# Performance work log

Measured on AMD Instinct MI355X. Metric: run time of the kernel, lower is better.

Reference implementation:

```python
import jax, jax.numpy as jnp
import numpy as np

NUM_ENTITIES = 40000
NUM_RELATIONS = 500
NUM_EDGES = 400000
ENT_DIM = 50
REL_DIM = 50
NUM_HEADS = 8
UNITS = [150, 300]
NEG_SLOPE = 0.2


def setup_inputs() -> dict:
    key = jax.random.key(0)
    ks = jax.random.split(key, 12)
    h_index = jax.random.randint(ks[0], (NUM_EDGES,), 0, NUM_ENTITIES)
    r_index = jax.random.randint(ks[1], (NUM_EDGES,), 0, NUM_RELATIONS)
    t_index = jax.random.randint(ks[2], (NUM_EDGES,), 0, NUM_ENTITIES)
    std_e = np.sqrt(1.0 / ENT_DIM).astype(np.float32)
    std_r = np.sqrt(1.0 / REL_DIM).astype(np.float32)
    entity_embeddings = jax.random.truncated_normal(ks[3], -2.0, 2.0, (NUM_ENTITIES, ENT_DIM), jnp.float32) * std_e
    relation_embeddings = jax.random.truncated_normal(ks[4], -2.0, 2.0, (NUM_RELATIONS, REL_DIM), jnp.float32) * std_r
    # gat0: input ent dim 50, rel dim 50 -> concat 150, units 150
    c0 = ENT_DIM + REL_DIM + ENT_DIM
    gat0_kernel = jax.random.normal(ks[5], (NUM_HEADS, c0, UNITS[0]), jnp.float32) * (1.0 / np.sqrt(c0))
    gat0_attn = jax.random.normal(ks[6], (NUM_HEADS, UNITS[0]), jnp.float32) * (1.0 / np.sqrt(UNITS[0]))
    gat0_rel_kernel = jax.random.normal(ks[7], (REL_DIM, UNITS[0]), jnp.float32) * (1.0 / np.sqrt(REL_DIM))
    # gat1: input ent dim 8*150=1200, rel dim 150 -> concat 2550, units 300
    e1 = NUM_HEADS * UNITS[0]
    c1 = e1 + UNITS[0] + e1
    gat1_kernel = jax.random.normal(ks[8], (NUM_HEADS, c1, UNITS[1]), jnp.float32) * (1.0 / np.sqrt(c1))
    gat1_attn = jax.random.normal(ks[9], (NUM_HEADS, UNITS[1]), jnp.float32) * (1.0 / np.sqrt(UNITS[1]))
    gat1_rel_kernel = jax.random.normal(ks[10], (UNITS[0], UNITS[1]), jnp.float32) * (1.0 / np.sqrt(UNITS[0]))
    dense_w = jax.random.normal(ks[11], (ENT_DIM, UNITS[1]), jnp.float32) * (1.0 / np.sqrt(ENT_DIM))
    dense_b = jnp.zeros((UNITS[1],), jnp.float32)
    return dict(h_index=h_index, r_index=r_index, t_index=t_index,
                entity_embeddings=entity_embeddings, relation_embeddings=relation_embeddings,
                gat0_kernel=gat0_kernel, gat0_attn=gat0_attn, gat0_rel_kernel=gat0_rel_kernel,
                gat1_kernel=gat1_kernel, gat1_attn=gat1_attn, gat1_rel_kernel=gat1_rel_kernel,
                dense_w=dense_w, dense_b=dense_b)


def _kbgat_layer(h, r, t, ent, rel, kernel, attn, rel_kernel):
    """One KBGAT layer. kernel: [H, De+Dr+De, U] acting on concat(ent[h], rel[r], ent[t]).
    Split kernel so projections happen at node/relation level (equivalent, avoids E x concat_dim)."""
    N = ent.shape[0]
    De = ent.shape[1]
    Dr = rel.shape[1]
    outs = []
    for hd in range(kernel.shape[0]):
        W = kernel[hd]
        Wh, Wr, Wt = W[:De], W[De:De + Dr], W[De + Dr:]
        # message c_{hrt} = W [ent_h ; rel_r ; ent_t] : [E, U]
        c = (ent @ Wh)[h] + (rel @ Wr)[r] + (ent @ Wt)[t]
        s = jax.nn.leaky_relu(c @ attn[hd], NEG_SLOPE)  # [E]
        # segment softmax over triples sharing the same head entity
        m = jax.ops.segment_max(s, h, num_segments=N)
        e = jnp.exp(s - m[h])
        d = jax.ops.segment_sum(e, h, num_segments=N)
        a = e / (d[h] + 1e-10)
        agg = jax.ops.segment_sum(a[:, None] * c, h, num_segments=N)  # [N, U]
        outs.append(jax.nn.elu(agg))
    rel_out = rel @ rel_kernel
    return outs, rel_out


def reference(h_index, r_index, t_index, entity_embeddings, relation_embeddings,
              gat0_kernel, gat0_attn, gat0_rel_kernel,
              gat1_kernel, gat1_attn, gat1_rel_kernel, dense_w, dense_b):
    h = h_index.astype(jnp.int32)
    r = r_index.astype(jnp.int32)
    t = t_index.astype(jnp.int32)
    # dropout rate is 0.0 / inference -> identity
    outs0, rel0 = _kbgat_layer(h, r, t, entity_embeddings, relation_embeddings,
                               gat0_kernel, gat0_attn, gat0_rel_kernel)
    feat = jnp.concatenate(outs0, axis=-1)  # [N, H*U0]
    outs1, rel1 = _kbgat_layer(h, r, t, feat, rel0, gat1_kernel, gat1_attn, gat1_rel_kernel)
    ent_out = outs1[0]
    for o in outs1[1:]:
        ent_out = ent_out + o  # add_n over heads
    ent_out = ent_out + (entity_embeddings @ dense_w + dense_b)  # dense residual
    return ent_out, rel1
```

## Files before the change

### kernel.cpp

```cpp
#include <hip/hip_runtime.h>
#include <hip/hip_bf16.h>
#include <math.h>
#include <stdint.h>

typedef __attribute__((ext_vector_type(8))) __bf16 bf16x8;
typedef __attribute__((ext_vector_type(4))) float f32x4;
typedef unsigned short us;

#define GLP(p) ((__attribute__((address_space(1))) void*)(p))
#define LDP(p) ((__attribute__((address_space(3))) void*)(p))

static __device__ __forceinline__ float b2f(us u) {
    return __uint_as_float(((unsigned int)u) << 16);
}
static __device__ __forceinline__ us f2b(float f) {
    unsigned int x = __float_as_uint(f);
    return (us)((x + 0x7fffu + ((x >> 16) & 1u)) >> 16);
}

__global__ __launch_bounds__(256) void sentinel(float* out, int n, float v) {
    int i = blockIdx.x * 256 + threadIdx.x;
    if (i < n) out[i] = v;
}

__global__ __launch_bounds__(256) void zero_featpad(us* __restrict__ feat) {
    int idx = blockIdx.x * 256 + threadIdx.x;
    if (idx < 40064 * 16) {
        int n = idx >> 4, c = idx & 15;
        feat[(size_t)n * 1216 + 1200 + c] = 0;
    }
}
__global__ __launch_bounds__(256) void zero_x0pad(us* __restrict__ X0) {
    int idx = blockIdx.x * 256 + threadIdx.x;
    if (idx < 4 * 64 * 192) {
        int w = idx / (64 * 192);
        int rem = idx % (64 * 192);
        int rr = rem / 192, c = rem % 192;
        X0[((size_t)w * 40064 + 40000 + rr) * 192 + c] = 0;
    }
}

__global__ __launch_bounds__(256) void count_edges(const int* __restrict__ h, int* __restrict__ counts) {
    int e = blockIdx.x * 256 + threadIdx.x;
    if (e < 400000) atomicAdd(&counts[h[e]], 1);
}

__global__ void scan40k(const int* __restrict__ counts, int* __restrict__ rs) {
    __shared__ int part[1024];
    int tid = threadIdx.x;
    int base = tid * 40;
    int s = 0;
    for (int i = 0; i < 40; ++i) { int idx = base + i; s += (idx < 40000) ? counts[idx] : 0; }
    part[tid] = s;
    __syncthreads();
    for (int off = 1; off < 1024; off <<= 1) {
        int v = (tid >= off) ? part[tid - off] : 0;
        __syncthreads();
        part[tid] += v;
        __syncthreads();
    }
    int run = (tid == 0) ? 0 : part[tid - 1];
    for (int i = 0; i < 40; ++i) {
        int idx = base + i;
        if (idx < 40000) { rs[idx] = run; run += counts[idx]; }
    }
    if (tid == 1023) rs[40000] = part[1023];
}

__global__ __launch_bounds__(256) void scatter_edges(const int* __restrict__ h, const int* __restrict__ rs,
                                                     int* __restrict__ cursor, int* __restrict__ se) {
    int e = blockIdx.x * 256 + threadIdx.x;
    if (e < 400000) {
        int n = h[e];
        int pos = rs[n] + atomicAdd(&cursor[n], 1);
        se[pos] = e;
    }
}

__global__ __launch_bounds__(256) void pack_ent(const float* __restrict__ ent, us* __restrict__ A0) {
    int idx = blockIdx.x * 256 + threadIdx.x;
    if (idx >= 40064 * 64) return;
    int n = idx >> 6, k = idx & 63;
    A0[idx] = (n < 40000 && k < 50) ? f2b(ent[n * 50 + k]) : (us)0;
}

__global__ __launch_bounds__(256) void build_V0(const float* __restrict__ g0k, const float* __restrict__ attn0,
                                                float* __restrict__ V0) {
    int idx = blockIdx.x * 256 + threadIdx.x;
    if (idx >= 50 * 24) return;
    int k = idx / 24, g = idx % 24;
    int part = g >> 3, hd = g & 7;
    int row = k + (part == 1 ? 100 : (part == 2 ? 50 : 0));
    float s = 0.f;
    for (int u = 0; u < 150; ++u)
        s += g0k[(hd * 150 + row) * 150 + u] * attn0[hd * 150 + u];
    V0[idx] = s;
}

__global__ __launch_bounds__(256) void build_VT0(const float* __restrict__ g0k, const float* __restrict__ attn0,
                                                 us* __restrict__ VT0) {
    int idx = blockIdx.x * 256 + threadIdx.x;
    if (idx >= 128 * 64) return;
    int g = idx >> 6, k = idx & 63;
    us v = 0;
    if (g < 16 && k < 50) {
        int part = g >> 3, hd = g & 7;
        int row = part ? (100 + k) : k;
        float s = 0.f;
        for (int u = 0; u < 150; ++u)
            s += g0k[(hd * 150 + row) * 150 + u] * attn0[hd * 150 + u];
        v = f2b(s);
    }
    VT0[idx] = v;
}

__global__ __launch_bounds__(256) void build_VT1(const float* __restrict__ g1k, const float* __restrict__ attn1,
                                                 us* __restrict__ VT1) {
    int idx = blockIdx.x * 256 + threadIdx.x;
    if (idx >= 128 * 1216) return;
    int g = idx / 1216, k = idx % 1216;
    us v = 0;
    if (g < 16 && k < 1200) {
        int part = g >> 3, hd = g & 7;
        int row = part ? (1350 + k) : k;
        float s = 0.f;
        for (int u = 0; u < 300; ++u)
            s += g1k[((size_t)hd * 2550 + row) * 300 + u] * attn1[hd * 300 + u];
        v = f2b(s);
    }
    VT1[idx] = v;
}

__global__ __launch_bounds__(256) void build_Vr1(const float* __restrict__ g1k, const float* __restrict__ attn1,
                                                 float* __restrict__ Vr1) {
    int idx = blockIdx.x * 256 + threadIdx.x;
    if (idx >= 150 * 8) return;
    int k = idx / 8, hd = idx % 8;
    float s = 0.f;
    for (int u = 0; u < 300; ++u)
        s += g1k[((size_t)hd * 2550 + 1200 + k) * 300 + u] * attn1[hd * 300 + u];
    Vr1[idx] = s;
}

__global__ __launch_bounds__(256) void scalar_proj(const void* __restrict__ Av, int aIsF32, int lda, int K,
                                                   const float* __restrict__ V, int ldv, int col0, int G,
                                                   float* __restrict__ out) {
    __shared__ float arow[1216];
    long n = blockIdx.x;
    if (aIsF32) {
        const float* A = (const float*)Av;
        for (int k = threadIdx.x; k < K; k += 256) arow[k] = A[n * lda + k];
    } else {
        const us* A = (const us*)Av;
        for (int k = threadIdx.x; k < K; k += 256) arow[k] = b2f(A[n * lda + k]);
    }
    __syncthreads();
    int g = threadIdx.x >> 4;
    int sl = threadIdx.x & 15;
    if (g < G) {
        float s = 0.f;
        for (int k = sl; k < K; k += 16) s += arow[k] * V[k * ldv + col0 + g];
        for (int off = 8; off; off >>= 1) s += __shfl_down(s, off, 16);
        if (sl == 0) out[n * G + g] = s;
    }
}

__global__ __launch_bounds__(256) void edge_stats(const int* __restrict__ rs, const int* __restrict__ se,
                                                  const int* __restrict__ rIdx, const int* __restrict__ tIdx,
                                                  const float* __restrict__ sc, const float* __restrict__ arr,
                                                  us* __restrict__ eAT, float* __restrict__ sfac) {
    int tid = blockIdx.x * 256 + threadIdx.x;
    if (tid >= 40000 * 8) return;
    int n = tid >> 3, hd = tid & 7;
    float ah = sc[n * 16 + hd];
    int p0 = rs[n], p1 = rs[n + 1];
    float m = -INFINITY, d = 0.f;
    for (int p = p0; p < p1; ++p) {
        int e = se[p];
        float s = ah + arr[rIdx[e] * 8 + hd] + sc[tIdx[e] * 16 + 8 + hd];
        s = (s > 0.f) ? s : 0.2f * s;
        if (s > m) { d = d * expf(m - s) + 1.f; m = s; }
        else d += expf(s - m);
    }
    float inv = 1.f / (d + 1e-10f);
    us* ea = eAT + (size_t)hd * 400000;
    for (int p = p0; p < p1; ++p) {
        int e = se[p];
        float s = ah + arr[rIdx[e] * 8 + hd] + sc[tIdx[e] * 16 + 8 + hd];
        s = (s > 0.f) ? s : 0.2f * s;
        ea[p] = f2b(expf(s - m) * inv);
    }
    sfac[tid] = d * inv;
}

__global__ __launch_bounds__(256) void agg0x4(int g, const int* __restrict__ rs, const int* __restrict__ se,
                                              const int* __restrict__ rIdx, const int* __restrict__ tIdx,
                                              const us* __restrict__ eAT, const float* __restrict__ sfac,
                                              const float* __restrict__ ent, const float* __restrict__ rel,
                                              us* __restrict__ X0) {
    __shared__ int sr[128], st[128];
    __shared__ float sa[4][128];
    long n = blockIdx.x;
    int tid = threadIdx.x;
    int lane = tid & 63, wave = tid >> 6;
    int hd = 4 * g + wave;
    int k = lane;
    float ev = (k < 50) ? ent[n * 50 + k] : 0.f;
    float xh = sfac[n * 8 + hd] * ev;
    float ra = 0.f, ta = 0.f;
    int p0 = rs[n], p1 = rs[n + 1];
    for (int c0 = p0; c0 < p1; c0 += 128) {
        int cnt = min(128, p1 - c0);
        __syncthreads();
        if (tid < cnt) {
            int e = se[c0 + tid];
            sr[tid] = rIdx[e];
            st[tid] = tIdx[e];
#pragma unroll
            for (int w = 0; w < 4; ++w)
                sa[w][tid] = b2f(eAT[(size_t)(4 * g + w) * 400000 + c0 + tid]);
        }
        __syncthreads();
#pragma unroll 2
        for (int i = 0; i < cnt; ++i) {
            float a = sa[wave][i];
            int r = sr[i], t = st[i];
            if (k < 50) {
                ra += a * rel[r * 50 + k];
                ta += a * ent[(long)t * 50 + k];
            }
        }
    }
    us* row = X0 + ((size_t)wave * 40064 + n) * 192;
    if (k < 50) { row[k] = f2b(xh); row[50 + k] = f2b(ra); row[100 + k] = f2b(ta); }
    if (lane < 42) row[150 + lane] = 0;
}

__global__ __launch_bounds__(256) void build_B0T8(const float* __restrict__ g0k, us* __restrict__ B) {
    int idx = blockIdx.x * 256 + threadIdx.x;
    if (idx >= 8 * 256 * 192) return;
    int hd = idx / (256 * 192);
    int u = (idx / 192) % 256, k = idx % 192;
    us v = 0;
    if (u < 150 && k < 150) v = f2b(g0k[((size_t)hd * 150 + k) * 150 + u]);
    B[idx] = v;
}

__global__ __launch_bounds__(256) void build_B1Th2(int g, const float* __restrict__ g1k, us* __restrict__ B) {
    int idx = blockIdx.x * 256 + threadIdx.x;
    if (idx >= 1280 * 1216) return;
    int j = idx / 1216, k = idx % 1216;
    us v = 0;
    if (j < 1216 && k < 1200) {
        int blk = j / 304, u = j % 304;
        if (u < 300) {
            int hd = 2 * g + (blk & 1);
            int row = (blk >= 2) ? (1350 + k) : k;
            v = f2b(g1k[((size_t)hd * 2550 + row) * 300 + u]);
        }
    }
    B[idx] = v;
}

__global__ __launch_bounds__(256) void gemm_bt(const us* __restrict__ A, const us* __restrict__ BT,
                                               us* __restrict__ C, int K, int ldc, int nColReal,
                                               int colOff0, int colOffZ, long aStrideZ, long btStrideZ,
                                               int act) {
    __shared__ __align__(16) us As[128 * 64];
    __shared__ __align__(16) us Bs[128 * 64];
    const int z = blockIdx.z;
    A += (size_t)z * aStrideZ;
    BT += (size_t)z * btStrideZ;
    const int colBase = colOff0 + z * colOffZ;
    const int tid = threadIdx.x;
    const int lane = tid & 63, wave = tid >> 6;
    const int wr = wave >> 1, wc = wave & 1;
    const int r16 = lane & 15, g4 = lane >> 4;
    const long bm = blockIdx.y, bn = blockIdx.x;
    const int cg = tid & 7;

    f32x4 acc[4][4];
#pragma unroll
    for (int m = 0; m < 4; ++m)
#pragma unroll
        for (int n = 0; n < 4; ++n) acc[m][n] = (f32x4){0.f, 0.f, 0.f, 0.f};

    for (int kt = 0; kt < K; kt += 64) {
#pragma unroll
        for (int i = 0; i < 4; ++i) {
            int idx = tid + i * 256;
            int row = idx >> 3;
            const us* ga = A + (bm * 128 + row) * (long)K + kt + cg * 8;
            __builtin_amdgcn_global_load_lds(GLP(ga), LDP(&As[idx * 8]), 16, 0, 0);
        }
#pragma unroll
        for (int i = 0; i < 4; ++i) {
            int idx = tid + i * 256;
            int row = idx >> 3;
            const us* gb = BT + (bn * 128 + row) * (long)K + kt + cg * 8;
            __builtin_amdgcn_global_load_lds(GLP(gb), LDP(&Bs[idx * 8]), 16, 0, 0);
        }
        asm volatile("s_waitcnt vmcnt(0)" ::: "memory");
        __syncthreads();
#pragma unroll
        for (int kk = 0; kk < 2; ++kk) {
            bf16x8 af[4], bfr[4];
#pragma unroll
            for (int m = 0; m < 4; ++m)
                af[m] = *(const bf16x8*)&As[(wr * 64 + m * 16 + r16) * 64 + kk * 32 + g4 * 8];
#pragma unroll
            for (int n = 0; n < 4; ++n)
                bfr[n] = *(const bf16x8*)&Bs[(wc * 64 + n * 16 + r16) * 64 + kk * 32 + g4 * 8];
#pragma unroll
            for (int m = 0; m < 4; ++m)
#pragma unroll
                for (int n = 0; n < 4; ++n)
                    acc[m][n] = __builtin_amdgcn_mfma_f32_16x16x32_bf16(af[m], bfr[n], acc[m][n], 0, 0, 0);
        }
        __syncthreads();
    }
#pragma unroll
    for (int m = 0; m < 4; ++m)
#pragma unroll
        for (int n = 0; n < 4; ++n)
#pragma unroll
            for (int j = 0; j < 4; ++j) {
                int cc = (int)bn * 128 + wc * 64 + n * 16 + r16;
                if (cc < nColReal) {
                    long row = bm * 128 + wr * 64 + m * 16 + g4 * 4 + j;
                    float v = acc[m][n][j];
                    if (act) v = (v > 0.f) ? v : expm1f(v);
                    C[row * (long)ldc + colBase + cc] = f2b(v);
                }
            }
}

__global__ __launch_bounds__(256) void gemm_bt_f32(const us* __restrict__ A, const us* __restrict__ BT,
                                                   float* __restrict__ C, int K, int ldc, int nColReal) {
    __shared__ __align__(16) us As[128 * 64];
    __shared__ __align__(16) us Bs[128 * 64];
    const int tid = threadIdx.x;
    const int lane = tid & 63, wave = tid >> 6;
    const int wr = wave >> 1, wc = wave & 1;
    const int r16 = lane & 15, g4 = lane >> 4;
    const long bm = blockIdx.y, bn = blockIdx.x;
    const int cg = tid & 7;

    f32x4 acc[4][4];
#pragma unroll
    for (int m = 0; m < 4; ++m)
#pragma unroll
        for (int n = 0; n < 4; ++n) acc[m][n] = (f32x4){0.f, 0.f, 0.f, 0.f};

    for (int kt = 0; kt < K; kt += 64) {
#pragma unroll
        for (int i = 0; i < 4; ++i) {
            int idx = tid + i * 256;
            int row = idx >> 3;
            const us* ga = A + (bm * 128 + row) * (long)K + kt + cg * 8;
            __builtin_amdgcn_global_load_lds(GLP(ga), LDP(&As[idx * 8]), 16, 0, 0);
        }
#pragma unroll
        for (int i = 0; i < 4; ++i) {
            int idx = tid + i * 256;
            int row = idx >> 3;
            const us* gb = BT + (bn * 128 + row) * (long)K + kt + cg * 8;
            __builtin_amdgcn_global_load_lds(GLP(gb), LDP(&Bs[idx * 8]), 16, 0, 0);
        }
        asm volatile("s_waitcnt vmcnt(0)" ::: "memory");
        __syncthreads();
#pragma unroll
        for (int kk = 0; kk < 2; ++kk) {
            bf16x8 af[4], bfr[4];
#pragma unroll
            for (int m = 0; m < 4; ++m)
                af[m] = *(const bf16x8*)&As[(wr * 64 + m * 16 + r16) * 64 + kk * 32 + g4 * 8];
#pragma unroll
            for (int n = 0; n < 4; ++n)
                bfr[n] = *(const bf16x8*)&Bs[(wc * 64 + n * 16 + r16) * 64 + kk * 32 + g4 * 8];
#pragma unroll
            for (int m = 0; m < 4; ++m)
#pragma unroll
                for (int n = 0; n < 4; ++n)
                    acc[m][n] = __builtin_amdgcn_mfma_f32_16x16x32_bf16(af[m], bfr[n], acc[m][n], 0, 0, 0);
        }
        __syncthreads();
    }
#pragma unroll
    for (int m = 0; m < 4; ++m)
#pragma unroll
        for (int n = 0; n < 4; ++n)
#pragma unroll
            for (int j = 0; j < 4; ++j) {
                int cc = (int)bn * 128 + wc * 64 + n * 16 + r16;
                if (cc < nColReal) {
                    long row = bm * 128 + wr * 64 + m * 16 + g4 * 4 + j;
                    C[row * (long)ldc + cc] = acc[m][n][j];
                }
            }
}

__global__ __launch_bounds__(256) void rel0_kernel(const float* __restrict__ rel, const float* __restrict__ g0rk,
                                                   float* __restrict__ rel0b) {
    int idx = blockIdx.x * 256 + threadIdx.x;
    if (idx >= 500 * 150) return;
    int rI = idx / 150, u = idx % 150;
    float s = 0.f;
    for (int k = 0; k < 50; ++k) s += rel[rI * 50 + k] * g0rk[k * 150 + u];
    rel0b[idx] = s;
}

__global__ __launch_bounds__(256) void pr1_kernel(const float* __restrict__ rel0b, const float* __restrict__ g1k,
                                                  float* __restrict__ PR1) {
    int idx = blockIdx.x * 256 + threadIdx.x;
    if (idx >= 500 * 2400) return;
    int rI = idx / 2400, jj = idx % 2400;
    int hd = jj / 300, u = jj % 300;
    float s = 0.f;
    for (int k = 0; k < 150; ++k)
        s += rel0b[rI * 150 + k] * g1k[((size_t)hd * 2550 + 1200 + k) * 300 + u];
    PR1[idx] = s;
}

__global__ __launch_bounds__(256) void rel1_kernel(const float* __restrict__ rel0b, const float* __restrict__ g1rk,
                                                   float* __restrict__ out) {
    int idx = blockIdx.x * 256 + threadIdx.x;
    if (idx >= 500 * 300) return;
    int rI = idx / 300, u = idx % 300;
    float s = 0.f;
    for (int k = 0; k < 150; ++k) s += rel0b[rI * 150 + k] * g1rk[k * 300 + u];
    out[idx] = s;
}

__global__ __launch_bounds__(256) void out_init(const float* __restrict__ ent, const float* __restrict__ dw,
                                                const float* __restrict__ db, float* __restrict__ outAcc) {
    int idx = blockIdx.x * 256 + threadIdx.x;
    if (idx >= 40000 * 300) return;
    int n = idx / 300, u = idx % 300;
    float s = db[u];
    for (int k = 0; k < 50; ++k) s += ent[n * 50 + k] * dw[k * 300 + u];
    outAcc[idx] = s;
}

__global__ __launch_bounds__(256) void agg1h2(int g, const int* __restrict__ rs, const int* __restrict__ se,
                                              const int* __restrict__ rIdx, const int* __restrict__ tIdx,
                                              const us* __restrict__ eAT, const float* __restrict__ sfac,
                                              const us* __restrict__ C1g2, const float* __restrict__ PR1,
                                              float* __restrict__ outf) {
    __shared__ int sr[128], st[128];
    __shared__ float sa0[128], sa1[128];
    long n = blockIdx.x;
    int tid = threadIdx.x;
    int hd0 = 2 * g, hd1 = hd0 + 1;
    int d = tid, d2 = tid + 256;
    bool a2 = (d2 < 300);
    float sf0 = sfac[n * 8 + hd0], sf1 = sfac[n * 8 + hd1];
    const us* crow = C1g2 + (size_t)n * 1216;
    float acc00 = sf0 * b2f(crow[d]);
    float acc10 = sf1 * b2f(crow[304 + d]);
    float acc01 = a2 ? sf0 * b2f(crow[d2]) : 0.f;
    float acc11 = a2 ? sf1 * b2f(crow[304 + d2]) : 0.f;
    const us* ea0 = eAT + (size_t)hd0 * 400000;
    const us* ea1 = eAT + (size_t)hd1 * 400000;
    int p0 = rs[n], p1 = rs[n + 1];
    for (int c0 = p0; c0 < p1; c0 += 128) {
        int cnt = min(128, p1 - c0);
        __syncthreads();
        if (tid < cnt) {
            int e = se[c0 + tid];
            sr[tid] = rIdx[e];
            st[tid] = tIdx[e];
            sa0[tid] = b2f(ea0[c0 + tid]);
            sa1[tid] = b2f(ea1[c0 + tid]);
        }
        __syncthreads();
#pragma unroll 2
        for (int i = 0; i < cnt; ++i) {
            int r = sr[i], t = st[i];
            float a0 = sa0[i], a1 = sa1[i];
            const us* ct = C1g2 + (size_t)t * 1216;
            const float* pr = PR1 + (size_t)r * 2400;
            acc00 += a0 * (pr[hd0 * 300 + d] + b2f(ct[608 + d]));
            acc10 += a1 * (pr[hd1 * 300 + d] + b2f(ct[912 + d]));
            if (a2) {
                acc01 += a0 * (pr[hd0 * 300 + d2] + b2f(ct[608 + d2]));
                acc11 += a1 * (pr[hd1 * 300 + d2] + b2f(ct[912 + d2]));
            }
        }
    }
    float v00 = (acc00 > 0.f) ? acc00 : expm1f(acc00);
    float v10 = (acc10 > 0.f) ? acc10 : expm1f(acc10);
    outf[n * 300 + d] += v00 + v10;
    if (a2) {
        float v01 = (acc01 > 0.f) ? acc01 : expm1f(acc01);
        float v11 = (acc11 > 0.f) ? acc11 : expm1f(acc11);
        outf[n * 300 + d2] += v01 + v11;
    }
}

extern "C" void kernel_launch(void* const* d_in, const int* in_sizes, int n_in,
                              void* d_out, int out_size, void* d_ws, size_t ws_size,
                              hipStream_t stream) {
    const int* hIdx = (const int*)d_in[0];
    const int* rIdx = (const int*)d_in[1];
    const int* tIdx = (const int*)d_in[2];
    const float* ent  = (const float*)d_in[3];
    const float* rel  = (const float*)d_in[4];
    const float* g0k  = (const float*)d_in[5];
    const float* at0w = (const float*)d_in[6];
    const float* g0rk = (const float*)d_in[7];
    const float* g1k  = (const float*)d_in[8];
    const float* at1w = (const float*)d_in[9];
    const float* g1rk = (const float*)d_in[10];
    const float* dw   = (const float*)d_in[11];
    const float* db   = (const float*)d_in[12];
    float* outf = (float*)d_out;

    {
        const int exp_sz[13] = {400000, 400000, 400000, 2000000, 25000, 180000, 1200,
                                7500, 6120000, 2400, 45000, 15000, 300};
        bool ok = (n_in == 13);
        for (int i = 0; ok && i < 13; ++i) ok = (in_sizes[i] == exp_sz[i]);
        if (!ok) {
            sentinel<<<(out_size + 255) / 256, 256, 0, stream>>>(outf, out_size, 44.0f);
            return;
        }
    }

    char* p = (char*)d_ws;
    auto carve = [&](size_t bytes) -> char* {
        char* r = p;
        p += (bytes + 255) & ~(size_t)255;
        return r;
    };
    int* counts = (int*)carve(40000 * 4);
    int* cursor = (int*)carve(40000 * 4);
    int* rs     = (int*)carve(40001 * 4);
    int* se     = (int*)carve(400000 * 4);
    float* sc   = (float*)carve((size_t)40064 * 16 * 4);
    float* arS  = (float*)carve(500 * 8 * 4);
    us* eAT     = (us*)carve((size_t)8 * 400000 * 2);
    float* sfac = (float*)carve((size_t)40000 * 8 * 4);
    float* V0  = (float*)carve(50 * 24 * 4);
    float* Vr1 = (float*)carve(150 * 8 * 4);
    float* rel0b = (float*)carve(500 * 150 * 4);
    float* PR1 = (float*)carve((size_t)500 * 2400 * 4);
    us* VT0   = (us*)carve((size_t)128 * 64 * 2);
    us* VT1   = (us*)carve((size_t)128 * 1216 * 2);
    us* B0T8  = (us*)carve((size_t)8 * 256 * 192 * 2);
    us* B1Th2 = (us*)carve((size_t)1280 * 1216 * 2);
    us* feat  = (us*)carve((size_t)40064 * 1216 * 2);
    char* tail = p;
    us* A0   = (us*)tail;
    us* X0   = (us*)tail;
    us* C1g2 = (us*)tail;
    size_t tailNeed = (size_t)40064 * 1216 * 2;
    size_t totalNeed = (size_t)(tail - (char*)d_ws) + tailNeed;
    if (totalNeed > ws_size) {
        sentinel<<<(out_size + 255) / 256, 256, 0, stream>>>(outf, out_size, 42.0f);
        return;
    }

    hipMemsetAsync(counts, 0, 40000 * 4, stream);
    hipMemsetAsync(cursor, 0, 40000 * 4, stream);
    zero_featpad<<<(40064 * 16 + 255) / 256, 256, 0, stream>>>(feat);

    count_edges<<<1563, 256, 0, stream>>>(hIdx, counts);
    scan40k<<<1, 1024, 0, stream>>>(counts, rs);
    scatter_edges<<<1563, 256, 0, stream>>>(hIdx, rs, cursor, se);

    pack_ent<<<(40064 * 64 + 255) / 256, 256, 0, stream>>>(ent, A0);
    build_VT0<<<(128 * 64 + 255) / 256, 256, 0, stream>>>(g0k, at0w, VT0);
    gemm_bt_f32<<<dim3(1, 313), 256, 0, stream>>>(A0, VT0, sc, 64, 16, 16);
    build_V0<<<5, 256, 0, stream>>>(g0k, at0w, V0);
    scalar_proj<<<500, 256, 0, stream>>>(rel, 1, 50, 50, V0, 24, 16, 8, arS);
    edge_stats<<<1250, 256, 0, stream>>>(rs, se, rIdx, tIdx, sc, arS, eAT, sfac);

    zero_x0pad<<<(4 * 64 * 192 + 255) / 256, 256, 0, stream>>>(X0);
    build_B0T8<<<(8 * 256 * 192 + 255) / 256, 256, 0, stream>>>(g0k, B0T8);
    for (int g = 0; g < 2; ++g) {
        agg0x4<<<40000, 256, 0, stream>>>(g, rs, se, rIdx, tIdx, eAT, sfac, ent, rel, X0);
        gemm_bt<<<dim3(2, 313, 4), 256, 0, stream>>>(X0, B0T8 + (size_t)g * 4 * 256 * 192, feat,
                                                     192, 1216, 150, g * 600, 150,
                                                     (long)40064 * 192, (long)256 * 192, 1);
    }

    rel0_kernel<<<(500 * 150 + 255) / 256, 256, 0, stream>>>(rel, g0rk, rel0b);
    build_VT1<<<(128 * 1216 + 255) / 256, 256, 0, stream>>>(g1k, at1w, VT1);
    build_Vr1<<<5, 256, 0, stream>>>(g1k, at1w, Vr1);
    gemm_bt_f32<<<dim3(1, 313), 256, 0, stream>>>(feat, VT1, sc, 1216, 16, 16);
    scalar_proj<<<500, 256, 0, stream>>>(rel0b, 1, 150, 150, Vr1, 8, 0, 8, arS);
    edge_stats<<<1250, 256, 0, stream>>>(rs, se, rIdx, tIdx, sc, arS, eAT, sfac);
    pr1_kernel<<<(500 * 2400 + 255) / 256, 256, 0, stream>>>(rel0b, g1k, PR1);

    out_init<<<(40000 * 300 + 255) / 256, 256, 0, stream>>>(ent, dw, db, outf);

    for (int g = 0; g < 4; ++g) {
        build_B1Th2<<<(1280 * 1216 + 255) / 256, 256, 0, stream>>>(g, g1k, B1Th2);
        gemm_bt<<<dim3(10, 313, 1), 256, 0, stream>>>(feat, B1Th2, C1g2,
                                                      1216, 1216, 1216, 0, 0, 0, 0, 0);
        agg1h2<<<40000, 256, 0, stream>>>(g, rs, se, rIdx, tIdx, eAT, sfac, C1g2, PR1, outf);
    }

    rel1_kernel<<<(500 * 300 + 255) / 256, 256, 0, stream>>>(rel0b, g1rk, outf + (size_t)40000 * 300);
}
```

Measured before the change: 2.333 ms.

## Double-buffer GEMM LDS tiles and XOR-swizzle layout to avoid bank conflicts

Both bf16 MFMA GEMM kernels now use two LDS buffers, so the global-to-LDS loads for the next K tile are issued before computing the current one, with a partial vmcnt wait. The LDS tile layout is also XOR-swizzled by row to reduce bank conflicts on the 16-byte fragment reads. The shared body is factored into a macro. This doubles LDS use per block (64KB), which may reduce occupancy.

```diff
diff --git a/kernel.cpp b/kernel.cpp
--- a/kernel.cpp
+++ b/kernel.cpp
@@ -262,142 +262,92 @@
     B[idx] = v;
 }
 
-__global__ __launch_bounds__(256) void gemm_bt(const us* __restrict__ A, const us* __restrict__ BT,
+#define GEMM_BODY(EPILOG)                                                                       \
+    __shared__ __align__(16) us As[2][128 * 64];                                                \
+    __shared__ __align__(16) us Bs[2][128 * 64];                                                \
+    const int tid = threadIdx.x;                                                                \
+    const int lane = tid & 63, wave = tid >> 6;                                                 \
+    const int wr = wave >> 1, wc = wave & 1;                                                    \
+    const int r16 = lane & 15, g4 = lane >> 4;                                                  \
+    const long bm = blockIdx.y, bn = blockIdx.x;                                                \
+    f32x4 acc[4][4];                                                                            \
+    _Pragma("unroll") for (int m = 0; m < 4; ++m)                                               \
+        _Pragma("unroll") for (int n = 0; n < 4; ++n) acc[m][n] = (f32x4){0.f, 0.f, 0.f, 0.f};  \
+    auto stage = [&](int buf, int kt) {                                                         \
+        _Pragma("unroll") for (int i = 0; i < 4; ++i) {                                         \
+            int idx = tid + i * 256;                                                            \
+            int row = idx >> 3, sub = idx & 7;                                                  \
+            int scol = ((sub ^ (row & 7)) << 3);                                                \
+            const us* ga = A + (bm * 128 + row) * (long)K + kt + scol;                          \
+            __builtin_amdgcn_global_load_lds(GLP(ga), LDP(&As[buf][idx * 8]), 16, 0, 0);        \
+        }                                                                                       \
+        _Pragma("unroll") for (int i = 0; i < 4; ++i) {                                         \
+            int idx = tid + i * 256;                                                            \
+            int row = idx >> 3, sub = idx & 7;                                                  \
+            int scol = ((sub ^ (row & 7)) << 3);                                                \
+            const us* gb = BT + (bn * 128 + row) * (long)K + kt + scol;                         \
+            __builtin_amdgcn_global_load_lds(GLP(gb), LDP(&Bs[buf][idx * 8]), 16, 0, 0);        \
+        }                                                                                       \
+    };                                                                                          \
+    const int nt = K >> 6;                                                                      \
+    stage(0, 0);                                                                                \
+    const int sxor = (r16 & 7) << 3;                                                            \
+    for (int t = 0; t < nt; ++t) {                                                              \
+        int cur = t & 1;                                                                        \
+        if (t + 1 < nt) {                                                                       \
+            stage(cur ^ 1, (t + 1) << 6);                                                       \
+            asm volatile("s_waitcnt vmcnt(8)" ::: "memory");                                    \
+        } else {                                                                                \
+            asm volatile("s_waitcnt vmcnt(0)" ::: "memory");                                    \
+        }                                                                                       \
+        __builtin_amdgcn_s_barrier();                                                           \
+        asm volatile("" ::: "memory");                                                          \
+        _Pragma("unroll") for (int kk = 0; kk < 2; ++kk) {                                      \
+            bf16x8 af[4], bfr[4];                                                               \
+            _Pragma("unroll") for (int m = 0; m < 4; ++m)                                       \
+                af[m] = *(const bf16x8*)&As[cur][(wr * 64 + m * 16 + r16) * 64 +                \
+                                               ((kk * 32 + g4 * 8) ^ sxor)];                    \
+            _Pragma("unroll") for (int n = 0; n < 4; ++n)                                       \
+                bfr[n] = *(const bf16x8*)&Bs[cur][(wc * 64 + n * 16 + r16) * 64 +               \
+                                                ((kk * 32 + g4 * 8) ^ sxor)];                   \
+            _Pragma("unroll") for (int m = 0; m < 4; ++m)                                       \
+                _Pragma("unroll") for (int n = 0; n < 4; ++n)                                   \
+                    acc[m][n] = __builtin_amdgcn_mfma_f32_16x16x32_bf16(af[m], bfr[n],          \
+                                                                        acc[m][n], 0, 0, 0);    \
+        }                                                                                       \
+        asm volatile("" ::: "memory");                                                          \
+        __builtin_amdgcn_s_barrier();                                                           \
+    }                                                                                           \
+    _Pragma("unroll") for (int m = 0; m < 4; ++m)                                               \
+        _Pragma("unroll") for (int n = 0; n < 4; ++n)                                           \
+            _Pragma("unroll") for (int j = 0; j < 4; ++j) { EPILOG }
+
+__global__ __launch_bounds__(256) void gemm_bt(const us* __restrict__ A_, const us* __restrict__ BT_,
                                                us* __restrict__ C, int K, int ldc, int nColReal,
                                                int colOff0, int colOffZ, long aStrideZ, long btStrideZ,
                                                int act) {
-    __shared__ __align__(16) us As[128 * 64];
-    __shared__ __align__(16) us Bs[128 * 64];
     const int z = blockIdx.z;
-    A += (size_t)z * aStrideZ;
-    BT += (size_t)z * btStrideZ;
+    const us* A = A_ + (size_t)z * aStrideZ;
+    const us* BT = BT_ + (size_t)z * btStrideZ;
     const int colBase = colOff0 + z * colOffZ;
-    const int tid = threadIdx.x;
-    const int lane = tid & 63, wave = tid >> 6;
-    const int wr = wave >> 1, wc = wave & 1;
-    const int r16 = lane & 15, g4 = lane >> 4;
-    const long bm = blockIdx.y, bn = blockIdx.x;
-    const int cg = tid & 7;
-
-    f32x4 acc[4][4];
-#pragma unroll
-    for (int m = 0; m < 4; ++m)
-#pragma unroll
-        for (int n = 0; n < 4; ++n) acc[m][n] = (f32x4){0.f, 0.f, 0.f, 0.f};
-
-    for (int kt = 0; kt < K; kt += 64) {
-#pragma unroll
-        for (int i = 0; i < 4; ++i) {
-            int idx = tid + i * 256;
-            int row = idx >> 3;
-            const us* ga = A + (bm * 128 + row) * (long)K + kt + cg * 8;
-            __builtin_amdgcn_global_load_lds(GLP(ga), LDP(&As[idx * 8]), 16, 0, 0);
-        }
-#pragma unroll
-        for (int i = 0; i < 4; ++i) {
-            int idx = tid + i * 256;
-            int row = idx >> 3;
-            const us* gb = BT + (bn * 128 + row) * (long)K + kt + cg * 8;
-            __builtin_amdgcn_global_load_lds(GLP(gb), LDP(&Bs[idx * 8]), 16, 0, 0);
-        }
-        asm volatile("s_waitcnt vmcnt(0)" ::: "memory");
-        __syncthreads();
-#pragma unroll
-        for (int kk = 0; kk < 2; ++kk) {
-            bf16x8 af[4], bfr[4];
-#pragma unroll
-            for (int m = 0; m < 4; ++m)
-                af[m] = *(const bf16x8*)&As[(wr * 64 + m * 16 + r16) * 64 + kk * 32 + g4 * 8];
-#pragma unroll
-            for (int n = 0; n < 4; ++n)
-                bfr[n] = *(const bf16x8*)&Bs[(wc * 64 + n * 16 + r16) * 64 + kk * 32 + g4 * 8];
-#pragma unroll
-            for (int m = 0; m < 4; ++m)
-#pragma unroll
-                for (int n = 0; n < 4; ++n)
-                    acc[m][n] = __builtin_amdgcn_mfma_f32_16x16x32_bf16(af[m], bfr[n], acc[m][n], 0, 0, 0);
-        }
-        __syncthreads();
-    }
-#pragma unroll
-    for (int m = 0; m < 4; ++m)
-#pragma unroll
-        for (int n = 0; n < 4; ++n)
-#pragma unroll
-            for (int j = 0; j < 4; ++j) {
-                int cc = (int)bn * 128 + wc * 64 + n * 16 + r16;
-                if (cc < nColReal) {
-                    long row = bm * 128 + wr * 64 + m * 16 + g4 * 4 + j;
-                    float v = acc[m][n][j];
-                    if (act) v = (v > 0.f) ? v : expm1f(v);
-                    C[row * (long)ldc + colBase + cc] = f2b(v);
-                }
-            }
+    GEMM_BODY(
+        int cc = (int)bn * 128 + wc * 64 + n * 16 + r16;
+        if (cc < nColReal) {
+            long row = bm * 128 + wr * 64 + m * 16 + g4 * 4 + j;
+            float v = acc[m][n][j];
+            if (act) v = (v > 0.f) ? v : expm1f(v);
+            C[row * (long)ldc + colBase + cc] = f2b(v);
+        })
 }
 
 __global__ __launch_bounds__(256) void gemm_bt_f32(const us* __restrict__ A, const us* __restrict__ BT,
                                                    float* __restrict__ C, int K, int ldc, int nColReal) {
-    __shared__ __align__(16) us As[128 * 64];
-    __shared__ __align__(16) us Bs[128 * 64];
-    const int tid = threadIdx.x;
-    const int lane = tid & 63, wave = tid >> 6;
-    const int wr = wave >> 1, wc = wave & 1;
-    const int r16 = lane & 15, g4 = lane >> 4;
-    const long bm = blockIdx.y, bn = blockIdx.x;
-    const int cg = tid & 7;
-
-    f32x4 acc[4][4];
-#pragma unroll
-    for (int m = 0; m < 4; ++m)
-#pragma unroll
-        for (int n = 0; n < 4; ++n) acc[m][n] = (f32x4){0.f, 0.f, 0.f, 0.f};
-
-    for (int kt = 0; kt < K; kt += 64) {
-#pragma unroll
-        for (int i = 0; i < 4; ++i) {
-            int idx = tid + i * 256;
-            int row = idx >> 3;
-            const us* ga = A + (bm * 128 + row) * (long)K + kt + cg * 8;
-            __builtin_amdgcn_global_load_lds(GLP(ga), LDP(&As[idx * 8]), 16, 0, 0);
-        }
-#pragma unroll
-        for (int i = 0; i < 4; ++i) {
-            int idx = tid + i * 256;
-            int row = idx >> 3;
-            const us* gb = BT + (bn * 128 + row) * (long)K + kt + cg * 8;
-            __builtin_amdgcn_global_load_lds(GLP(gb), LDP(&Bs[idx * 8]), 16, 0, 0);
-        }
-        asm volatile("s_waitcnt vmcnt(0)" ::: "memory");
-        __syncthreads();
-#pragma unroll
-        for (int kk = 0; kk < 2; ++kk) {
-            bf16x8 af[4], bfr[4];
-#pragma unroll
-            for (int m = 0; m < 4; ++m)
-                af[m] = *(const bf16x8*)&As[(wr * 64 + m * 16 + r16) * 64 + kk * 32 + g4 * 8];
-#pragma unroll
-            for (int n = 0; n < 4; ++n)
-                bfr[n] = *(const bf16x8*)&Bs[(wc * 64 + n * 16 + r16) * 64 + kk * 32 + g4 * 8];
-#pragma unroll
-            for (int m = 0; m < 4; ++m)
-#pragma unroll
-                for (int n = 0; n < 4; ++n)
-                    acc[m][n] = __builtin_amdgcn_mfma_f32_16x16x32_bf16(af[m], bfr[n], acc[m][n], 0, 0, 0);
-        }
-        __syncthreads();
-    }
-#pragma unroll
-    for (int m = 0; m < 4; ++m)
-#pragma unroll
-        for (int n = 0; n < 4; ++n)
-#pragma unroll
-            for (int j = 0; j < 4; ++j) {
-                int cc = (int)bn * 128 + wc * 64 + n * 16 + r16;
-                if (cc < nColReal) {
-                    long row = bm * 128 + wr * 64 + m * 16 + g4 * 4 + j;
-                    C[row * (long)ldc + cc] = acc[m][n][j];
-                }
-            }
+    GEMM_BODY(
+        int cc = (int)bn * 128 + wc * 64 + n * 16 + r16;
+        if (cc < nColReal) {
+            long row = bm * 128 + wr * 64 + m * 16 + g4 * 4 + j;
+            C[row * (long)ldc + cc] = acc[m][n][j];
+        })
 }
 
 __global__ __launch_bounds__(256) void rel0_kernel(const float* __restrict__ rel, const float* __restrict__ g0rk,
```

Result: faster. 2.191 ms (-6.1%).
